# Kernel tuning notes

Measured on AMD Instinct MI355X. Metric: run time of the kernel, lower is better.

## Reference

```python
import jax, jax.numpy as jnp
import numpy as np

N, D, K = 32768, 256, 8192
SQRT3 = 3.0 ** 0.5


def setup_inputs() -> dict:
    key = jax.random.key(0)
    k1, k2 = jax.random.split(key)
    x = jax.random.normal(k1, (N, D), dtype=jnp.float32)
    # torch .uniform_(-sqrt(3), sqrt(3)) on an [D, K] table
    embeddings = jax.random.uniform(k2, (D, K), dtype=jnp.float32,
                                    minval=-SQRT3, maxval=SQRT3)
    return {"x": x, "embeddings": embeddings}


def reference(x, embeddings):
    # x: [N, D] (forward flattens from dim 1; 2D input is identity)
    # embeddings: [D, K]
    # squared L2 distances: ||y||^2 - 2 y.E + ||e||^2  -> [N, K]
    dist = (jnp.sum(x * x, axis=1, keepdims=True)
            - 2.0 * (x @ embeddings)
            + jnp.sum(embeddings * embeddings, axis=0, keepdims=True))
    idx = jnp.argmin(dist, axis=1)  # [N]
    # one_hot(idx) @ E^T == gather of columns of E (same math, no dense one-hot)
    quantized = jnp.take(embeddings, idx, axis=1).T  # [N, D]
    return quantized.reshape(x.shape)
```

## Files before the change

### kernel.cpp

```cpp
#include <hip/hip_runtime.h>
#include <math.h>
#include <float.h>

#define N_ROWS 32768
#define D_DIM  256
#define K_DIM  8192

#define EPS1 0.25f
#define EPS2 0.02f
#define T2CAP 4096
#define T3CAP 512
#define NSPLIT3 16

typedef _Float16 f16;
typedef _Float16 f16x8 __attribute__((ext_vector_type(8)));
typedef float f32x4 __attribute__((ext_vector_type(4)));

#define KSPLIT 8
#define COLS_PER_SPLIT (K_DIM / KSPLIT)
#define CHUNK_COLS 32
#define NCHUNK (COLS_PER_SPLIT / CHUNK_COLS)
#define CHUNK_BYTES (CHUNK_COLS * D_DIM * 2)

typedef unsigned int u32;
typedef const u32 __attribute__((address_space(1)))* gas1_u32;
typedef u32 __attribute__((address_space(3)))* las3_u32;
__device__ __forceinline__ void gload_lds16(const void* g, void* l) {
    __builtin_amdgcn_global_load_lds((gas1_u32)g, (las3_u32)l, 16, 0, 0);
}

__global__ void convx_kernel(const float* __restrict__ X, f16* __restrict__ X16) {
    const size_t i = ((size_t)blockIdx.x * 256 + threadIdx.x) * 8;
    float4 a = *reinterpret_cast<const float4*>(X + i);
    float4 b = *reinterpret_cast<const float4*>(X + i + 4);
    f16x8 o;
    o[0]=(f16)a.x; o[1]=(f16)a.y; o[2]=(f16)a.z; o[3]=(f16)a.w;
    o[4]=(f16)b.x; o[5]=(f16)b.y; o[6]=(f16)b.z; o[7]=(f16)b.w;
    *reinterpret_cast<f16x8*>(X16 + i) = o;
}

__global__ void transpose_kernel(const float* __restrict__ E, float* __restrict__ ET) {
    __shared__ float t[64][65];
    const int bk = blockIdx.x & (K_DIM / 64 - 1);
    const int bd = blockIdx.x >> 7;
    const int c  = threadIdx.x & 63;
    const int r0 = (threadIdx.x >> 6) * 16;
    const int d0 = bd * 64, k0 = bk * 64;
#pragma unroll
    for (int i = 0; i < 16; ++i)
        t[r0 + i][c] = E[(size_t)(d0 + r0 + i) * K_DIM + k0 + c];
    __syncthreads();
#pragma unroll
    for (int i = 0; i < 16; ++i)
        ET[(size_t)(k0 + r0 + i) * D_DIM + d0 + c] = t[c][r0 + i];
}

__global__ void packe_et_kernel(const float* __restrict__ ET, f16* __restrict__ Epack) {
    const int gid = blockIdx.x * 256 + threadIdx.x;
    const int l    = gid & 63;
    const int t    = (gid >> 6) & 7;
    const int tile = gid >> 9;
    const int k  = 16 * tile + (l & 15);
    const int d0 = 32 * t + (l >> 4) * 8;
    float4 a = *reinterpret_cast<const float4*>(&ET[(size_t)k * D_DIM + d0]);
    float4 b = *reinterpret_cast<const float4*>(&ET[(size_t)k * D_DIM + d0 + 4]);
    f16x8 o;
    o[0]=(f16)a.x; o[1]=(f16)a.y; o[2]=(f16)a.z; o[3]=(f16)a.w;
    o[4]=(f16)b.x; o[5]=(f16)b.y; o[6]=(f16)b.z; o[7]=(f16)b.w;
    *reinterpret_cast<f16x8*>(Epack + (size_t)gid * 8) = o;
}

__global__ void packe_kernel(const float* __restrict__ E, f16* __restrict__ Epack) {
    const int gid = blockIdx.x * 256 + threadIdx.x;
    const int l    = gid & 63;
    const int t    = (gid >> 6) & 7;
    const int tile = gid >> 9;
    const int k  = 16 * tile + (l & 15);
    const int d0 = 32 * t + (l >> 4) * 8;
    f16x8 o;
#pragma unroll
    for (int j = 0; j < 8; ++j) o[j] = (f16)E[(size_t)(d0 + j) * K_DIM + k];
    *reinterpret_cast<f16x8*>(Epack + (size_t)gid * 8) = o;
}

__global__ void nhen_kernel(const float* __restrict__ E, float* __restrict__ nhen) {
    const int k = blockIdx.x * 256 + threadIdx.x;
    float s = 0.0f;
#pragma unroll 8
    for (int d = 0; d < D_DIM; ++d) {
        float v = E[(size_t)d * K_DIM + k];
        s = fmaf(v, v, s);
    }
    nhen[k] = -0.5f * s;
}

__launch_bounds__(256, 2)
__global__ void pass1_kernel(const f16* __restrict__ X16,
                             const f16* __restrict__ Epack,
                             const float* __restrict__ nhen,
                             float* __restrict__ p_best,
                             float* __restrict__ p_sec,
                             int*   __restrict__ p_idx) {
    __shared__ f16 B_lds[3][CHUNK_BYTES / 2];
    __shared__ float nh_lds[COLS_PER_SPLIT];

    const int tid = threadIdx.x;
    const int wv = tid >> 6;
    const int lane = tid & 63;
    const int l15 = lane & 15;
    const int l4  = lane >> 4;
    const int rg = blockIdx.x >> 3;
    const int ks = blockIdx.x & 7;
    const int rowW = rg * 256 + wv * 64;
    const int colBase = ks * COLS_PER_SPLIT;

    f16x8 A[4][8];
#pragma unroll
    for (int rt = 0; rt < 4; ++rt)
#pragma unroll
        for (int t = 0; t < 8; ++t)
            A[rt][t] = *reinterpret_cast<const f16x8*>(
                X16 + (size_t)(rowW + 16*rt + l15) * D_DIM + 32*t + l4*8);

    *reinterpret_cast<float4*>(&nh_lds[tid * 4]) =
        *reinterpret_cast<const float4*>(nhen + colBase + tid * 4);

    float best[16], sec[16];
    int bbase[16];
#pragma unroll
    for (int s = 0; s < 16; ++s) { best[s] = -INFINITY; sec[s] = -INFINITY; bbase[s] = 0; }

    const char* splitSrc = (const char*)Epack + (size_t)colBase * 512;

    auto STAGE = [&](int buf, int ci) {
        const char* csrc = splitSrc + (size_t)ci * CHUNK_BYTES;
        char* cdst = (char*)&B_lds[buf][0];
#pragma unroll
        for (int c = 0; c < 4; ++c) {
            const int seg = wv * 4 + c;
            gload_lds16(csrc + seg * 1024 + (lane << 4), cdst + seg * 1024);
        }
    };

    auto COMPUTE = [&](int bi, int ci) {
        const f16* bufc = &B_lds[bi][0];
        const int c0 = colBase + ci * CHUNK_COLS;
#pragma unroll
        for (int ct = 0; ct < 2; ++ct) {
            const float nh = nh_lds[ci * CHUNK_COLS + ct * 16 + l15];
            const f32x4 nh4 = {nh, nh, nh, nh};
            f32x4 acc[4];
            {
                f16x8 B = *reinterpret_cast<const f16x8*>(bufc + (ct*8)*512 + lane*8);
#pragma unroll
                for (int rt = 0; rt < 4; ++rt)
                    acc[rt] = __builtin_amdgcn_mfma_f32_16x16x32_f16(A[rt][0], B, nh4, 0, 0, 0);
            }
#pragma unroll
            for (int t = 1; t < 8; ++t) {
                f16x8 B = *reinterpret_cast<const f16x8*>(bufc + (ct*8 + t)*512 + lane*8);
#pragma unroll
                for (int rt = 0; rt < 4; ++rt)
                    acc[rt] = __builtin_amdgcn_mfma_f32_16x16x32_f16(A[rt][t], B, acc[rt], 0, 0, 0);
            }
#pragma unroll
            for (int rt = 0; rt < 4; ++rt) {
#pragma unroll
                for (int r = 0; r < 4; ++r) {
                    const float v = acc[rt][r];
                    const int sl = rt*4 + r;
                    sec[sl] = __builtin_amdgcn_fmed3f(v, best[sl], sec[sl]);
                    const bool gt = v > best[sl];
                    best[sl] = gt ? v : best[sl];
                    bbase[sl] = gt ? (c0 + 16*ct) : bbase[sl];
                }
            }
        }
    };

    STAGE(0, 0);
    STAGE(1, 1);
    asm volatile("s_waitcnt lgkmcnt(0)" ::: "memory");

    int cur = 0;
    for (int ci = 0; ci < NCHUNK - 1; ++ci) {
        asm volatile("s_waitcnt vmcnt(4)" ::: "memory");
        __builtin_amdgcn_s_barrier();
        if (ci + 2 < NCHUNK) {
            int nb = cur + 2; if (nb >= 3) nb -= 3;
            STAGE(nb, ci + 2);
        }
        COMPUTE(cur, ci);
        cur = (cur + 1 == 3) ? 0 : cur + 1;
    }
    asm volatile("s_waitcnt vmcnt(0)" ::: "memory");
    __builtin_amdgcn_s_barrier();
    COMPUTE(cur, NCHUNK - 1);

#pragma unroll
    for (int s = 0; s < 16; ++s) {
        float b = best[s], sc = sec[s];
        int k = bbase[s] + l15;
#pragma unroll
        for (int off = 8; off >= 1; off >>= 1) {
            float ob = __shfl_xor(b, off, 16);
            float os = __shfl_xor(sc, off, 16);
            int   ok = __shfl_xor(k, off, 16);
            float sm = fmaxf(fmaxf(sc, os), fminf(b, ob));
            bool take = (ob > b) || (ob == b && ok < k);
            b = take ? ob : b;
            k = take ? ok : k;
            sc = sm;
        }
        if (l15 == 0) {
            const int row = rowW + 16*(s >> 2) + 4*l4 + (s & 3);
            p_best[ks * N_ROWS + row] = b;
            p_sec [ks * N_ROWS + row] = sc;
            p_idx [ks * N_ROWS + row] = k;
        }
    }
}

__global__ void zero_counts_kernel(int* count, int* count3) { *count = 0; *count3 = 0; }

__global__ void merge_kernel(const float* __restrict__ p_best,
                             const float* __restrict__ p_sec,
                             const int*   __restrict__ p_idx,
                             int* __restrict__ idxf,
                             int* __restrict__ list, int* __restrict__ count) {
    const int n = blockIdx.x * 256 + threadIdx.x;
    float b = p_best[n], sc = p_sec[n];
    int k = p_idx[n];
#pragma unroll
    for (int s = 1; s < KSPLIT; ++s) {
        float ob = p_best[s * N_ROWS + n];
        float os = p_sec [s * N_ROWS + n];
        int   ok = p_idx [s * N_ROWS + n];
        float sm = fmaxf(fmaxf(sc, os), fminf(b, ob));
        bool take = ob > b;
        b = take ? ob : b; k = take ? ok : k; sc = sm;
    }
    idxf[n] = k;
    if (2.0f * (b - sc) < EPS1) {
        int pos = atomicAdd(count, 1);
        if (pos < T2CAP) list[pos] = n;
    }
}

__launch_bounds__(256, 2)
__global__ void tier2_kernel(const float* __restrict__ X,
                             const float* __restrict__ E,
                             const float* __restrict__ nhen,
                             const int* __restrict__ list,
                             const int* __restrict__ count,
                             float* __restrict__ t2b, float* __restrict__ t2s,
                             int* __restrict__ t2i) {
    const int g  = blockIdx.x >> 4;
    const int sp = blockIdx.x & 15;
    const int cnt = min(*count, T2CAP);
    if (g * 64 >= cnt) return;

    __shared__ float xT[D_DIM][64];
    __shared__ float es[64][64];
    const int tid = threadIdx.x;
    const int tx = tid & 15, ty = tid >> 4;

    {
        const int r = tid >> 2;
        const int slot = min(g * 64 + r, cnt - 1);
        const int row = list[slot];
        const int d0 = (tid & 3) * 64;
        const float* xp = X + (size_t)row * D_DIM + d0;
#pragma unroll
        for (int i = 0; i < 64; i += 4) {
            float4 v = *reinterpret_cast<const float4*>(xp + i);
            xT[d0+i+0][r] = v.x; xT[d0+i+1][r] = v.y;
            xT[d0+i+2][r] = v.z; xT[d0+i+3][r] = v.w;
        }
    }

    float best[4], sec[4]; int bidx[4];
#pragma unroll
    for (int i = 0; i < 4; ++i) { best[i] = -INFINITY; sec[i] = -INFINITY; bidx[i] = 0; }

    const int colBase = sp * 512;
    for (int kc = 0; kc < 512; kc += 64) {
        float acc[4][4];
#pragma unroll
        for (int i = 0; i < 4; ++i)
#pragma unroll
            for (int j = 0; j < 4; ++j) acc[i][j] = 0.0f;

        for (int dc = 0; dc < D_DIM; dc += 64) {
            __syncthreads();
#pragma unroll
            for (int dd = 0; dd < 64; dd += 16) {
                int d = dd + (tid >> 4);
                float4 v = *reinterpret_cast<const float4*>(
                    &E[(size_t)(dc + d) * K_DIM + colBase + kc + (tid & 15) * 4]);
                *reinterpret_cast<float4*>(&es[d][(tid & 15) * 4]) = v;
            }
            __syncthreads();
#pragma unroll 8
            for (int d = 0; d < 64; ++d) {
                float4 xv = *reinterpret_cast<const float4*>(&xT[dc + d][ty * 4]);
                float4 ev = *reinterpret_cast<const float4*>(&es[d][tx * 4]);
                float xr[4] = {xv.x, xv.y, xv.z, xv.w};
                float ec[4] = {ev.x, ev.y, ev.z, ev.w};
#pragma unroll
                for (int i = 0; i < 4; ++i)
#pragma unroll
                    for (int j = 0; j < 4; ++j)
                        acc[i][j] = fmaf(xr[i], ec[j], acc[i][j]);
            }
        }
        float4 nhv = *reinterpret_cast<const float4*>(&nhen[colBase + kc + tx * 4]);
        float nh[4] = {nhv.x, nhv.y, nhv.z, nhv.w};
#pragma unroll
        for (int j = 0; j < 4; ++j) {
            const int k = colBase + kc + tx * 4 + j;
#pragma unroll
            for (int i = 0; i < 4; ++i) {
                float u = nh[j] + acc[i][j];
                bool gt = u > best[i];
                sec[i]  = fmaxf(sec[i], fminf(u, best[i]));
                best[i] = gt ? u : best[i];
                bidx[i] = gt ? k : bidx[i];
            }
        }
    }

#pragma unroll
    for (int off = 8; off >= 1; off >>= 1) {
#pragma unroll
        for (int i = 0; i < 4; ++i) {
            float ob = __shfl_xor(best[i], off, 16);
            float os = __shfl_xor(sec[i], off, 16);
            int   ok = __shfl_xor(bidx[i], off, 16);
            float sm = fmaxf(fmaxf(sec[i], os), fminf(best[i], ob));
            bool take = (ob > best[i]) || (ob == best[i] && ok < bidx[i]);
            best[i] = take ? ob : best[i];
            bidx[i] = take ? ok : bidx[i];
            sec[i] = sm;
        }
    }
    if (tx == 0) {
#pragma unroll
        for (int i = 0; i < 4; ++i) {
            const int slot = g * 64 + ty * 4 + i;
            if (slot < cnt) {
                t2b[sp * T2CAP + slot] = best[i];
                t2s[sp * T2CAP + slot] = sec[i];
                t2i[sp * T2CAP + slot] = bidx[i];
            }
        }
    }
}

__global__ void merge2_kernel(const float* __restrict__ t2b,
                              const float* __restrict__ t2s,
                              const int*   __restrict__ t2i,
                              const int* __restrict__ list,
                              const int* __restrict__ count,
                              int* __restrict__ idxf,
                              int* __restrict__ list3, int* __restrict__ count3) {
    const int slot = blockIdx.x * 256 + threadIdx.x;
    const int cnt = min(*count, T2CAP);
    if (slot >= cnt) return;
    float b = t2b[slot], sc = t2s[slot];
    int k = t2i[slot];
#pragma unroll
    for (int sp = 1; sp < 16; ++sp) {
        float ob = t2b[sp * T2CAP + slot];
        float os = t2s[sp * T2CAP + slot];
        int   ok = t2i[sp * T2CAP + slot];
        float sm = fmaxf(fmaxf(sc, os), fminf(b, ob));
        bool take = ob > b;
        b = take ? ob : b; k = take ? ok : k; sc = sm;
    }
    const int n = list[slot];
    idxf[n] = k;
    if (2.0f * (b - sc) < EPS2) {
        int pos = atomicAdd(count3, 1);
        if (pos < T3CAP) list3[pos] = n;
    }
}

__launch_bounds__(256)
__global__ void tier3_kernel(const float* __restrict__ X,
                             const float* __restrict__ E,
                             const int* __restrict__ list3,
                             const int* __restrict__ count3,
                             double* __restrict__ t3b, int* __restrict__ t3i) {
    const int slot = blockIdx.x >> 4;
    const int sp   = blockIdx.x & 15;
    const int cnt = min(*count3, T3CAP);
    if (slot >= cnt) return;
    const int n = list3[slot];

    __shared__ float xs[D_DIM];
    const int tid = threadIdx.x;
    xs[tid] = X[(size_t)n * D_DIM + tid];
    __syncthreads();

    const int colBase = sp * 512;
    double best = DBL_MAX;
    int bi = 0x7fffffff;
#pragma unroll
    for (int kk = 0; kk < 512; kk += 256) {
        const int k = colBase + kk + tid;
        double s0 = 0.0, s1 = 0.0, s2 = 0.0, s3 = 0.0;
#pragma unroll 4
        for (int d = 0; d < D_DIM; d += 4) {
            double f0 = (double)xs[d+0] - (double)E[(size_t)(d+0) * K_DIM + k];
            double f1 = (double)xs[d+1] - (double)E[(size_t)(d+1) * K_DIM + k];
            double f2 = (double)xs[d+2] - (double)E[(size_t)(d+2) * K_DIM + k];
            double f3 = (double)xs[d+3] - (double)E[(size_t)(d+3) * K_DIM + k];
            s0 = fma(f0, f0, s0); s1 = fma(f1, f1, s1);
            s2 = fma(f2, f2, s2); s3 = fma(f3, f3, s3);
        }
        double s = (s0 + s1) + (s2 + s3);
        if (s < best) { best = s; bi = k; }
    }

    __shared__ double bv[256];
    __shared__ int bix[256];
    bv[tid] = best; bix[tid] = bi;
    __syncthreads();
    if (tid == 0) {
        double b = bv[0]; int ix = bix[0];
        for (int t = 1; t < 256; ++t)
            if (bv[t] < b || (bv[t] == b && bix[t] < ix)) { b = bv[t]; ix = bix[t]; }
        t3b[sp * T3CAP + slot] = b;
        t3i[sp * T3CAP + slot] = ix;
    }
}

__global__ void merge3_kernel(const double* __restrict__ t3b,
                              const int* __restrict__ t3i,
                              const int* __restrict__ list3,
                              const int* __restrict__ count3,
                              int* __restrict__ idxf) {
    const int slot = blockIdx.x * 256 + threadIdx.x;
    const int cnt = min(*count3, T3CAP);
    if (slot >= cnt) return;
    double b = t3b[slot];
    int k = t3i[slot];
#pragma unroll
    for (int sp = 1; sp < NSPLIT3; ++sp) {
        double ob = t3b[sp * T3CAP + slot];
        int   ok = t3i[sp * T3CAP + slot];
        if (ob < b || (ob == b && ok < k)) { b = ob; k = ok; }
    }
    idxf[list3[slot]] = k;
}

__global__ void gather2_kernel(const float* __restrict__ ET,
                               const int* __restrict__ idx,
                               float* __restrict__ out) {
    const int n  = blockIdx.x * 4 + (threadIdx.x >> 6);
    const int d4 = (threadIdx.x & 63) * 4;
    const int k  = idx[n];
    *reinterpret_cast<float4*>(&out[(size_t)n * D_DIM + d4]) =
        *reinterpret_cast<const float4*>(&ET[(size_t)k * D_DIM + d4]);
}

__global__ void gather_kernel(const float* __restrict__ E,
                              const int* __restrict__ idx,
                              float* __restrict__ out) {
    const int n = blockIdx.x;
    const int d = threadIdx.x;
    const int k = idx[n];
    out[(size_t)n * D_DIM + d] = E[(size_t)d * K_DIM + k];
}

__global__ void fb_enorm_kernel(const float* __restrict__ E, float* __restrict__ enorm) {
    int k = blockIdx.x * 256 + threadIdx.x;
    float s = 0.0f;
#pragma unroll 8
    for (int d = 0; d < D_DIM; ++d) { float v = E[(size_t)d * K_DIM + k]; s = fmaf(v, v, s); }
    enorm[k] = s;
}

__launch_bounds__(256, 2)
__global__ void fb_dist_kernel(const float* __restrict__ X, const float* __restrict__ E,
                               const float* __restrict__ enorm,
                               int* __restrict__ idx_out, float* __restrict__ gap_out) {
    __shared__ float xT[D_DIM][64];
    __shared__ float es[64][64];
    const int tid = threadIdx.x;
    const int tx = tid & 15, ty = tid >> 4;
    const int rowBase = blockIdx.x * 64;
    {
        const int r = tid >> 2;
        const int d0 = (tid & 3) * 64;
        const float* xp = X + (size_t)(rowBase + r) * D_DIM + d0;
#pragma unroll
        for (int i = 0; i < 64; i += 4) {
            float4 v = *reinterpret_cast<const float4*>(xp + i);
            xT[d0+i+0][r]=v.x; xT[d0+i+1][r]=v.y; xT[d0+i+2][r]=v.z; xT[d0+i+3][r]=v.w;
        }
    }
    float bestVal[4], secVal[4]; int bestIdx[4];
#pragma unroll
    for (int i = 0; i < 4; ++i) { bestVal[i]=INFINITY; secVal[i]=INFINITY; bestIdx[i]=0; }
    for (int kc = 0; kc < K_DIM; kc += 64) {
        float acc[4][4];
#pragma unroll
        for (int i=0;i<4;++i)
#pragma unroll
            for (int j=0;j<4;++j) acc[i][j]=0.f;
        for (int dc = 0; dc < D_DIM; dc += 64) {
            __syncthreads();
#pragma unroll
            for (int dd = 0; dd < 64; dd += 16) {
                int d = dd + (tid >> 4);
                float4 v = *reinterpret_cast<const float4*>(
                    &E[(size_t)(dc+d)*K_DIM + kc + (tid&15)*4]);
                *reinterpret_cast<float4*>(&es[d][(tid&15)*4]) = v;
            }
            __syncthreads();
#pragma unroll 8
            for (int d = 0; d < 64; ++d) {
                float4 xv = *reinterpret_cast<const float4*>(&xT[dc+d][ty*4]);
                float4 ev = *reinterpret_cast<const float4*>(&es[d][tx*4]);
                float xr[4]={xv.x,xv.y,xv.z,xv.w}, ec[4]={ev.x,ev.y,ev.z,ev.w};
#pragma unroll
                for (int i=0;i<4;++i)
#pragma unroll
                    for (int j=0;j<4;++j) acc[i][j]=fmaf(xr[i],ec[j],acc[i][j]);
            }
        }
        float4 env = *reinterpret_cast<const float4*>(&enorm[kc + tx*4]);
        float en[4]={env.x,env.y,env.z,env.w};
#pragma unroll
        for (int j=0;j<4;++j) {
            int k = kc + tx*4 + j;
#pragma unroll
            for (int i=0;i<4;++i) {
                float s = fmaf(-2.0f, acc[i][j], en[j]);
                if (s < bestVal[i]) { secVal[i]=bestVal[i]; bestVal[i]=s; bestIdx[i]=k; }
                else if (s < secVal[i]) secVal[i]=s;
            }
        }
    }
#pragma unroll
    for (int off=8; off>=1; off>>=1) {
#pragma unroll
        for (int i=0;i<4;++i) {
            float oB=__shfl_xor(bestVal[i],off,16);
            int oI=__shfl_xor(bestIdx[i],off,16);
            float oS=__shfl_xor(secVal[i],off,16);
            float ms=fminf(fminf(secVal[i],oS),fmaxf(bestVal[i],oB));
            if (oB<bestVal[i] || (oB==bestVal[i] && oI<bestIdx[i])) { bestVal[i]=oB; bestIdx[i]=oI; }
            secVal[i]=ms;
        }
    }
    if (tx==0) {
#pragma unroll
        for (int i=0;i<4;++i) {
            idx_out[rowBase + ty*4 + i] = bestIdx[i];
            gap_out[rowBase + ty*4 + i] = secVal[i]-bestVal[i];
        }
    }
}

__launch_bounds__(256)
__global__ void fb_refine_kernel(const float* __restrict__ X, const float* __restrict__ E,
                                 const float* __restrict__ gap, int* __restrict__ idx) {
    const int n = blockIdx.x;
    if (gap[n] >= 0.0625f) return;
    __shared__ float xs[D_DIM];
    const int tid = threadIdx.x;
    xs[tid] = X[(size_t)n * D_DIM + tid];
    __syncthreads();
    double best = DBL_MAX; int bi = 0x7fffffff;
    for (int k = tid; k < K_DIM; k += 256) {
        double s0=0,s1=0,s2=0,s3=0;
#pragma unroll 4
        for (int d = 0; d < D_DIM; d += 4) {
            double f0=(double)xs[d+0]-(double)E[(size_t)(d+0)*K_DIM+k];
            double f1=(double)xs[d+1]-(double)E[(size_t)(d+1)*K_DIM+k];
            double f2=(double)xs[d+2]-(double)E[(size_t)(d+2)*K_DIM+k];
            double f3=(double)xs[d+3]-(double)E[(size_t)(d+3)*K_DIM+k];
            s0=fma(f0,f0,s0); s1=fma(f1,f1,s1); s2=fma(f2,f2,s2); s3=fma(f3,f3,s3);
        }
        double s=(s0+s1)+(s2+s3);
        if (s<best){best=s;bi=k;}
    }
    __shared__ double bv[256]; __shared__ int bix[256];
    bv[tid]=best; bix[tid]=bi;
    __syncthreads();
    if (tid==0) {
        double b=bv[0]; int ix=bix[0];
        for (int t=1;t<256;++t)
            if (bv[t]<b || (bv[t]==b && bix[t]<ix)) { b=bv[t]; ix=bix[t]; }
        idx[n]=ix;
    }
}

extern "C" void kernel_launch(void* const* d_in, const int* in_sizes, int n_in,
                              void* d_out, int out_size, void* d_ws, size_t ws_size,
                              hipStream_t stream) {
    const float* X = (const float*)d_in[0];
    const float* E = (const float*)d_in[1];
    float* out = (float*)d_out;
    char* ws = (char*)d_ws;

    const size_t o_nhen  = 0;
    const size_t o_pb    = 32768;
    const size_t o_ps    = o_pb  + (size_t)KSPLIT * N_ROWS * 4;
    const size_t o_pi    = o_ps  + (size_t)KSPLIT * N_ROWS * 4;
    const size_t o_idx   = o_pi  + (size_t)KSPLIT * N_ROWS * 4;
    const size_t o_list  = o_idx + (size_t)N_ROWS * 4;
    const size_t o_count = o_list + (size_t)T2CAP * 4;
    const size_t o_t2b   = o_count + 256;
    const size_t o_t2s   = o_t2b + (size_t)16 * T2CAP * 4;
    const size_t o_t2i   = o_t2s + (size_t)16 * T2CAP * 4;
    const size_t o_list3 = o_t2i + (size_t)16 * T2CAP * 4;
    const size_t o_t3b   = o_list3 + (size_t)T3CAP * 4;
    const size_t o_t3i   = o_t3b + (size_t)NSPLIT3 * T3CAP * 8;
    const size_t o_x16   = o_t3i + (size_t)NSPLIT3 * T3CAP * 4;
    const size_t o_epack = o_x16 + (size_t)N_ROWS * D_DIM * 2;
    const size_t NEED_BASE = o_epack + (size_t)D_DIM * K_DIM * 2;
    const size_t o_et    = NEED_BASE;
    const size_t NEED_FULL = o_et + (size_t)D_DIM * K_DIM * 4;

    if (ws_size >= NEED_BASE) {
        float*  nhen  = (float*) (ws + o_nhen);
        float*  p_b   = (float*) (ws + o_pb);
        float*  p_s   = (float*) (ws + o_ps);
        int*    p_i   = (int*)   (ws + o_pi);
        int*    idxf  = (int*)   (ws + o_idx);
        int*    list  = (int*)   (ws + o_list);
        int*    count = (int*)   (ws + o_count);
        int*    count3= (int*)   (ws + o_count + 4);
        float*  t2b   = (float*) (ws + o_t2b);
        float*  t2s   = (float*) (ws + o_t2s);
        int*    t2i   = (int*)   (ws + o_t2i);
        int*    list3 = (int*)   (ws + o_list3);
        double* t3b   = (double*)(ws + o_t3b);
        int*    t3i   = (int*)   (ws + o_t3i);
        f16*    X16   = (f16*)   (ws + o_x16);
        f16*    Epack = (f16*)   (ws + o_epack);
        float*  ET    = (float*) (ws + o_et);
        const bool haveET = ws_size >= NEED_FULL;

        convx_kernel<<<(N_ROWS * D_DIM / 8) / 256, 256, 0, stream>>>(X, X16);
        if (haveET) {
            transpose_kernel<<<(K_DIM / 64) * (D_DIM / 64), 256, 0, stream>>>(E, ET);
            packe_et_kernel<<<(K_DIM / 16) * 8 * 64 / 256, 256, 0, stream>>>(ET, Epack);
        } else {
            packe_kernel<<<(K_DIM / 16) * 8 * 64 / 256, 256, 0, stream>>>(E, Epack);
        }
        nhen_kernel<<<K_DIM / 256, 256, 0, stream>>>(E, nhen);
        zero_counts_kernel<<<1, 1, 0, stream>>>(count, count3);
        pass1_kernel<<<(N_ROWS / 256) * KSPLIT, 256, 0, stream>>>(
            X16, Epack, nhen, p_b, p_s, p_i);
        merge_kernel<<<N_ROWS / 256, 256, 0, stream>>>(
            p_b, p_s, p_i, idxf, list, count);
        tier2_kernel<<<(T2CAP / 64) * 16, 256, 0, stream>>>(
            X, E, nhen, list, count, t2b, t2s, t2i);
        merge2_kernel<<<T2CAP / 256, 256, 0, stream>>>(
            t2b, t2s, t2i, list, count, idxf, list3, count3);
        tier3_kernel<<<T3CAP * NSPLIT3, 256, 0, stream>>>(
            X, E, list3, count3, t3b, t3i);
        merge3_kernel<<<T3CAP / 256, 256, 0, stream>>>(
            t3b, t3i, list3, count3, idxf);
        if (haveET)
            gather2_kernel<<<N_ROWS / 4, 256, 0, stream>>>(ET, idxf, out);
        else
            gather_kernel<<<N_ROWS, 256, 0, stream>>>(E, idxf, out);
    } else {
        float* enorm = (float*)ws;
        int*   idx   = (int*)(ws + 32768);
        float* gap   = (float*)(ws + 32768 + (size_t)N_ROWS * 4);
        fb_enorm_kernel<<<K_DIM / 256, 256, 0, stream>>>(E, enorm);
        fb_dist_kernel<<<N_ROWS / 64, 256, 0, stream>>>(X, E, enorm, idx, gap);
        fb_refine_kernel<<<N_ROWS, 256, 0, stream>>>(X, E, gap, idx);
        gather_kernel<<<N_ROWS, 256, 0, stream>>>(E, idx, out);
    }
}
```

Measured before the change: 325.2 us.

## Software-pipeline argmin scoring of previous tile with MFMA of current tile

Splits the chunk compute into per-16-column tiles with two ping-pong accumulator sets, so the best/second-best scoring of the previous tile is interleaved with the MFMA chain of the current tile. The goal is to hide the VALU argmax/median work and the MFMA result latency behind matrix instructions instead of running them serially after each tile. The final chunk is folded into the main loop with a trailing epilogue that scores the last tile. This costs more live registers for the second accumulator set, which may lower occupancy or cause spills.

```diff
diff --git a/kernel.cpp b/kernel.cpp
--- a/kernel.cpp
+++ b/kernel.cpp
@@ -142,37 +142,34 @@
         }
     };
 
-    auto COMPUTE = [&](int bi, int ci) {
-        const f16* bufc = &B_lds[bi][0];
-        const int c0 = colBase + ci * CHUNK_COLS;
-#pragma unroll
-        for (int ct = 0; ct < 2; ++ct) {
-            const float nh = nh_lds[ci * CHUNK_COLS + ct * 16 + l15];
-            const f32x4 nh4 = {nh, nh, nh, nh};
-            f32x4 acc[4];
-            {
-                f16x8 B = *reinterpret_cast<const f16x8*>(bufc + (ct*8)*512 + lane*8);
+    f32x4 accA[4], accB[4];
+    int cA = 0, cB = 0;
+
+    auto TILE = [&](const f16* bufc, int ct, int nhoff,
+                    f32x4 (&accN)[4], f32x4 (&accP)[4], int cP, bool doScore) {
+        const float nh = nh_lds[nhoff + l15];
+        const f32x4 nh4 = {nh, nh, nh, nh};
+#pragma unroll
+        for (int t = 0; t < 8; ++t) {
+            f16x8 B = *reinterpret_cast<const f16x8*>(bufc + (ct*8 + t)*512 + lane*8);
+            if (t == 0) {
 #pragma unroll
                 for (int rt = 0; rt < 4; ++rt)
-                    acc[rt] = __builtin_amdgcn_mfma_f32_16x16x32_f16(A[rt][0], B, nh4, 0, 0, 0);
-            }
-#pragma unroll
-            for (int t = 1; t < 8; ++t) {
-                f16x8 B = *reinterpret_cast<const f16x8*>(bufc + (ct*8 + t)*512 + lane*8);
+                    accN[rt] = __builtin_amdgcn_mfma_f32_16x16x32_f16(A[rt][0], B, nh4, 0, 0, 0);
+            } else {
 #pragma unroll
                 for (int rt = 0; rt < 4; ++rt)
-                    acc[rt] = __builtin_amdgcn_mfma_f32_16x16x32_f16(A[rt][t], B, acc[rt], 0, 0, 0);
-            }
-#pragma unroll
-            for (int rt = 0; rt < 4; ++rt) {
-#pragma unroll
-                for (int r = 0; r < 4; ++r) {
-                    const float v = acc[rt][r];
-                    const int sl = rt*4 + r;
-                    sec[sl] = __builtin_amdgcn_fmed3f(v, best[sl], sec[sl]);
-                    const bool gt = v > best[sl];
-                    best[sl] = gt ? v : best[sl];
-                    bbase[sl] = gt ? (c0 + 16*ct) : bbase[sl];
+                    accN[rt] = __builtin_amdgcn_mfma_f32_16x16x32_f16(A[rt][t], B, accN[rt], 0, 0, 0);
+            }
+            if (doScore) {
+#pragma unroll
+                for (int s = 2*t; s <= 2*t + 1; ++s) {
+                    const int rt2 = s >> 2, r2 = s & 3;
+                    const float v = accP[rt2][r2];
+                    sec[s] = __builtin_amdgcn_fmed3f(v, best[s], sec[s]);
+                    const bool gt = v > best[s];
+                    best[s] = gt ? v : best[s];
+                    bbase[s] = gt ? cP : bbase[s];
                 }
             }
         }
@@ -183,19 +180,37 @@
     asm volatile("s_waitcnt lgkmcnt(0)" ::: "memory");
 
     int cur = 0;
-    for (int ci = 0; ci < NCHUNK - 1; ++ci) {
-        asm volatile("s_waitcnt vmcnt(4)" ::: "memory");
+    for (int ci = 0; ci < NCHUNK; ++ci) {
+        if (ci < NCHUNK - 1) {
+            asm volatile("s_waitcnt vmcnt(4)" ::: "memory");
+        } else {
+            asm volatile("s_waitcnt vmcnt(0)" ::: "memory");
+        }
         __builtin_amdgcn_s_barrier();
         if (ci + 2 < NCHUNK) {
             int nb = cur + 2; if (nb >= 3) nb -= 3;
             STAGE(nb, ci + 2);
         }
-        COMPUTE(cur, ci);
+        const f16* bufc = &B_lds[cur][0];
+        const int base = colBase + ci * CHUNK_COLS;
+        if (ci == 0) {
+            TILE(bufc, 0, ci*32,      accA, accB, cB, false); cA = base;
+            TILE(bufc, 1, ci*32 + 16, accB, accA, cA, true);  cB = base + 16;
+        } else {
+            TILE(bufc, 0, ci*32,      accA, accB, cB, true);  cA = base;
+            TILE(bufc, 1, ci*32 + 16, accB, accA, cA, true);  cB = base + 16;
+        }
         cur = (cur + 1 == 3) ? 0 : cur + 1;
     }
-    asm volatile("s_waitcnt vmcnt(0)" ::: "memory");
-    __builtin_amdgcn_s_barrier();
-    COMPUTE(cur, NCHUNK - 1);
+#pragma unroll
+    for (int s = 0; s < 16; ++s) {
+        const int rt2 = s >> 2, r2 = s & 3;
+        const float v = accB[rt2][r2];
+        sec[s] = __builtin_amdgcn_fmed3f(v, best[s], sec[s]);
+        const bool gt = v > best[s];
+        best[s] = gt ? v : best[s];
+        bbase[s] = gt ? cB : bbase[s];
+    }
 
 #pragma unroll
     for (int s = 0; s < 16; ++s) {
```

Result: no change. 324.3 us (-0.3%).
